# Kernel optimization log

Measured on AMD Instinct MI355X. Metric: run time of the kernel, lower is better.

Reference implementation:

```python
import jax, jax.numpy as jnp
import numpy as np

N_REP = 8      # N: repeated gelu(LN(linear)) blocks
M_LAYERS = 4   # M: transformer encoder layers
SEQ = 100
D = 4
FF = 2048      # PyTorch TransformerEncoderLayer default dim_feedforward
H = 4          # nhead; head_dim = 1


def _ln(x, g, b, axes):
    m = jnp.mean(x, axis=axes, keepdims=True)
    v = jnp.var(x, axis=axes, keepdims=True)
    return (x - m) / jnp.sqrt(v + 1e-5) * g + b


def _encoder_layer(x, Win, bi, Wout, bout, W1, b1, W2, b2, g1, be1, g2, be2):
    # x: [S, Nb, D] with S = batch_size (batch_first=False!), Nb = 100
    S, Nb, E = x.shape
    qkv = x @ Win.T + bi                      # [S, Nb, 3D]
    q, k, v = jnp.split(qkv, 3, axis=-1)
    qh = q.reshape(S, Nb, H, E // H)          # head_dim = 1, scale 1/sqrt(1)=1
    kh = k.reshape(S, Nb, H, E // H)
    vh = v.reshape(S, Nb, H, E // H)
    scores = jnp.einsum('snhd,tnhd->nhst', qh, kh)   # [Nb, H, S, S]
    attn = jax.nn.softmax(scores, axis=-1)
    o = jnp.einsum('nhst,tnhd->snhd', attn, vh).reshape(S, Nb, E)
    o = o @ Wout.T + bout
    x = _ln(x + o, g1, be1, (-1,))            # post-norm (norm_first=False)
    f = jax.nn.relu(x @ W1.T + b1) @ W2.T + b2
    return _ln(x + f, g2, be2, (-1,))


def setup_inputs() -> dict:
    key = jax.random.key(0)
    ks = jax.random.split(key, 24)
    B = 256
    d = {}
    d['x'] = jax.random.normal(ks[0], (B, SEQ, D), dtype=jnp.float32)
    # conv1: kernel_size=1, 1->1 channel -> scalar affine
    d['conv_w'] = jax.random.normal(ks[1], (), dtype=jnp.float32) * 0.5 + 1.0
    d['conv_b'] = jax.random.normal(ks[2], (), dtype=jnp.float32) * 0.1
    # shared 4x4 linear (self.liner) and LayerNorm([100,4])
    d['Wl'] = jax.random.normal(ks[3], (D, D), dtype=jnp.float32) * 0.5
    d['bl'] = jax.random.normal(ks[4], (D,), dtype=jnp.float32) * 0.1
    d['ln_g'] = jnp.ones((SEQ, D), dtype=jnp.float32)
    d['ln_b'] = jnp.zeros((SEQ, D), dtype=jnp.float32)
    # transformer encoder params, stacked over M layers
    s = 0.3
    d['Win'] = jax.random.normal(ks[5], (M_LAYERS, 3 * D, D), dtype=jnp.float32) * s
    d['bi'] = jax.random.normal(ks[6], (M_LAYERS, 3 * D), dtype=jnp.float32) * 0.05
    d['Wout'] = jax.random.normal(ks[7], (M_LAYERS, D, D), dtype=jnp.float32) * s
    d['bout'] = jax.random.normal(ks[8], (M_LAYERS, D), dtype=jnp.float32) * 0.05
    d['W1'] = jax.random.normal(ks[9], (M_LAYERS, FF, D), dtype=jnp.float32) * 0.05
    d['b1'] = jax.random.normal(ks[10], (M_LAYERS, FF), dtype=jnp.float32) * 0.05
    d['W2'] = jax.random.normal(ks[11], (M_LAYERS, D, FF), dtype=jnp.float32) * 0.02
    d['b2'] = jax.random.normal(ks[12], (M_LAYERS, D), dtype=jnp.float32) * 0.05
    d['g1'] = jnp.ones((M_LAYERS, D), dtype=jnp.float32)
    d['be1'] = jnp.zeros((M_LAYERS, D), dtype=jnp.float32)
    d['g2'] = jnp.ones((M_LAYERS, D), dtype=jnp.float32)
    d['be2'] = jnp.zeros((M_LAYERS, D), dtype=jnp.float32)
    return d


def reference(x, conv_w, conv_b, Wl, bl, ln_g, ln_b,
              Win, bi, Wout, bout, W1, b1, W2, b2, g1, be1, g2, be2):
    # per-channel kernel_size=1 conv == elementwise affine (same scalar for all 4 channels)
    h = x * conv_w + conv_b                   # [B, 100, 4]
    for _ in range(N_REP):
        h = jax.nn.gelu(_ln(h @ Wl.T + bl, ln_g, ln_b, (-2, -1)), approximate=False)
    h = h @ Wl.T + bl
    for i in range(M_LAYERS):
        h = _encoder_layer(h, Win[i], bi[i], Wout[i], bout[i], W1[i], b1[i],
                           W2[i], b2[i], g1[i], be1[i], g2[i], be2[i])
    h = h @ Wl.T + bl
    return jax.nn.softmax(h, axis=2)
```

## Files before the change

kernel.cpp:

```cpp
#include <hip/hip_runtime.h>
#include <math.h>

#define SEQ   100
#define BATCH 256
#define NREP  8
#define FFD   2048
#define RSQRT2 0.70710678118654752440f

__device__ __forceinline__ float wsum(float v) {
#pragma unroll
  for (int o = 32; o > 0; o >>= 1) v += __shfl_xor(v, o, 64);
  return v;
}

__global__ __launch_bounds__(256) void k_prep(
    const float* __restrict__ W2, float* __restrict__ W2T)
{
  const int id = blockIdx.x * 256 + threadIdx.x;
  const float* src = W2 + (id >> 11) * 4 * FFD + (id & 2047);
  *(float4*)(W2T + id * 4) =
      make_float4(src[0], src[FFD], src[2 * FFD], src[3 * FFD]);
}

__global__ __launch_bounds__(64) void k_stageA(
    const float* __restrict__ x, const float* __restrict__ convw,
    const float* __restrict__ convb, const float* __restrict__ Wl,
    const float* __restrict__ bl, const float* __restrict__ lng,
    const float* __restrict__ lnb, float* __restrict__ XT)
{
  const int b = blockIdx.x;
  const int lane = threadIdx.x;
  const bool act = lane < 50;

  const float cw = convw[0], cb = convb[0];
  float W[4][4], B[4];
#pragma unroll
  for (int j = 0; j < 4; ++j) {
    B[j] = bl[j];
#pragma unroll
    for (int d = 0; d < 4; ++d) W[j][d] = Wl[j * 4 + d];
  }
  float h[2][4] = {{0.f,0.f,0.f,0.f},{0.f,0.f,0.f,0.f}};
  float gg[2][4] = {{0.f}}, eb[2][4] = {{0.f}};
  if (act) {
#pragma unroll
    for (int p = 0; p < 2; ++p) {
      const int r = lane * 2 + p;
      float4 xr = *(const float4*)(x + (b * SEQ + r) * 4);
      h[p][0] = fmaf(xr.x, cw, cb); h[p][1] = fmaf(xr.y, cw, cb);
      h[p][2] = fmaf(xr.z, cw, cb); h[p][3] = fmaf(xr.w, cw, cb);
      float4 gv = *(const float4*)(lng + r * 4);
      float4 bv = *(const float4*)(lnb + r * 4);
      gg[p][0] = gv.x; gg[p][1] = gv.y; gg[p][2] = gv.z; gg[p][3] = gv.w;
      eb[p][0] = bv.x; eb[p][1] = bv.y; eb[p][2] = bv.z; eb[p][3] = bv.w;
    }
  }
  for (int it = 0; it < NREP; ++it) {
    float y[2][4] = {{0.f,0.f,0.f,0.f},{0.f,0.f,0.f,0.f}};
    float s1 = 0.f, s2 = 0.f;
    if (act) {
#pragma unroll
      for (int p = 0; p < 2; ++p)
#pragma unroll
        for (int j = 0; j < 4; ++j) {
          float yy = B[j];
#pragma unroll
          for (int d = 0; d < 4; ++d) yy = fmaf(h[p][d], W[j][d], yy);
          y[p][j] = yy; s1 += yy; s2 = fmaf(yy, yy, s2);
        }
    }
    s1 = wsum(s1); s2 = wsum(s2);
    const float mean = s1 * (1.0f / 400.0f);
    const float var  = s2 * (1.0f / 400.0f) - mean * mean;
    const float rstd = rsqrtf(var + 1e-5f);
    if (act) {
#pragma unroll
      for (int p = 0; p < 2; ++p)
#pragma unroll
        for (int j = 0; j < 4; ++j) {
          float vv = fmaf((y[p][j] - mean) * rstd, gg[p][j], eb[p][j]);
          h[p][j] = 0.5f * vv * (1.0f + erff(vv * RSQRT2));
        }
    }
  }
  if (act) {
#pragma unroll
    for (int p = 0; p < 2; ++p) {
      const int r = lane * 2 + p;
      float yy[4];
#pragma unroll
      for (int j = 0; j < 4; ++j) {
        float a = B[j];
#pragma unroll
        for (int d = 0; d < 4; ++d) a = fmaf(h[p][d], W[j][d], a);
        yy[j] = a;
      }
      *(float4*)(XT + (r * BATCH + b) * 4) =
          make_float4(yy[0], yy[1], yy[2], yy[3]);
    }
  }
}

__global__ __launch_bounds__(1024, 4) void k_layer(
    const float* __restrict__ XTin, float* __restrict__ XTout,
    const float* __restrict__ Wa,  const float* __restrict__ ba,
    const float* __restrict__ Wo,  const float* __restrict__ bo,
    const float* __restrict__ W1l, const float* __restrict__ b1l,
    const float* __restrict__ W2Tl,const float* __restrict__ b2l,
    const float* __restrict__ g1l, const float* __restrict__ e1l,
    const float* __restrict__ g2l, const float* __restrict__ e2l,
    const float* __restrict__ Wl,  const float* __restrict__ bl,
    float* __restrict__ out, const int last)
{
  const int n      = blockIdx.x;
  const int base_s = blockIdx.y * 128;
  const int t      = threadIdx.x;
  const int lane   = t & 63;
  const int wv     = t >> 6;
  const int ah     = wv & 3;
  const int kq     = wv >> 2;

  __shared__ __align__(16) float2 kv[4][256];
  __shared__ float2 part[4][128][5];
  __shared__ float  osm[4][128];
  __shared__ float  x1s[128][4];
  __shared__ float  fout[128][4];
  __shared__ float2 kred[4][4];

  {
    const int s = t & 255, hh = t >> 8;
    float4 xr = *(const float4*)(XTin + (n * BATCH + s) * 4);
    const float* wk = Wa + (4 + hh) * 4;
    const float* wp = Wa + (8 + hh) * 4;
    float k = ba[4+hh] + xr.x*wk[0] + xr.y*wk[1] + xr.z*wk[2] + xr.w*wk[3];
    float v = ba[8+hh] + xr.x*wp[0] + xr.y*wp[1] + xr.z*wp[2] + xr.w*wp[3];
    kv[hh][s] = make_float2(k, v);
  }
  float q0, q1;
  {
    const float* wq = Wa + ah * 4;
    float4 xa = *(const float4*)(XTin + (n * BATCH + base_s + 2 * lane) * 4);
    float4 xb = *(const float4*)(XTin + (n * BATCH + base_s + 2 * lane + 1) * 4);
    q0 = ba[ah] + xa.x*wq[0] + xa.y*wq[1] + xa.z*wq[2] + xa.w*wq[3];
    q1 = ba[ah] + xb.x*wq[0] + xb.y*wq[1] + xb.z*wq[2] + xb.w*wq[3];
  }
  __syncthreads();

  {
    float k = kv[ah][kq * 64 + lane].x;
    float mx = k, mn = k;
#pragma unroll
    for (int o = 32; o > 0; o >>= 1) {
      mx = fmaxf(mx, __shfl_xor(mx, o, 64));
      mn = fminf(mn, __shfl_xor(mn, o, 64));
    }
    if (lane == 0) kred[ah][kq] = make_float2(mx, mn);
  }
  __syncthreads();

  {
    const float kmx = fmaxf(fmaxf(kred[ah][0].x, kred[ah][1].x),
                            fmaxf(kred[ah][2].x, kred[ah][3].x));
    const float kmn = fminf(fminf(kred[ah][0].y, kred[ah][1].y),
                            fminf(kred[ah][2].y, kred[ah][3].y));
    const float m0 = (q0 >= 0.f) ? q0 * kmx : q0 * kmn;
    const float m1 = (q1 >= 0.f) ? q1 * kmx : q1 * kmn;
    const int kb = kq * 64;
    float dA = 0.f, nA = 0.f, dB = 0.f, nB = 0.f;
#pragma unroll 4
    for (int i = 0; i < 32; ++i) {
      const int p = ((lane + i) & 31) * 2;
      float4 kk = *(const float4*)&kv[ah][kb + p];
      float pA0 = __expf(fmaf(q0, kk.x, -m0));
      float pA1 = __expf(fmaf(q0, kk.z, -m0));
      float pB0 = __expf(fmaf(q1, kk.x, -m1));
      float pB1 = __expf(fmaf(q1, kk.z, -m1));
      dA += pA0 + pA1; nA = fmaf(pA1, kk.w, fmaf(pA0, kk.y, nA));
      dB += pB0 + pB1; nB = fmaf(pB1, kk.w, fmaf(pB0, kk.y, nB));
    }
    part[ah][2 * lane][kq]     = make_float2(dA, nA);
    part[ah][2 * lane + 1][kq] = make_float2(dB, nB);
  }
  __syncthreads();

  if (t < 512) {
    const int h = t >> 7, qr = t & 127;
    float2 a = part[h][qr][0], b = part[h][qr][1];
    float2 c = part[h][qr][2], d = part[h][qr][3];
    osm[h][qr] = (a.y + b.y + c.y + d.y) / (a.x + b.x + c.x + d.x);
  }
  __syncthreads();

  if (t < 512) {
    const int r = t >> 2, d = t & 3;
    const float o0 = osm[0][r], o1 = osm[1][r], o2 = osm[2][r], o3 = osm[3][r];
    float rr = XTin[(n * BATCH + base_s + r) * 4 + d] + bo[d]
             + o0*Wo[d*4+0] + o1*Wo[d*4+1] + o2*Wo[d*4+2] + o3*Wo[d*4+3];
    float sum = rr + __shfl_xor(rr, 1, 64); sum += __shfl_xor(sum, 2, 64);
    const float mean = 0.25f * sum;
    const float dv = rr - mean;
    float qq = dv * dv;
    float qs = qq + __shfl_xor(qq, 1, 64); qs += __shfl_xor(qs, 2, 64);
    const float rstd = rsqrtf(0.25f * qs + 1e-5f);
    x1s[r][d] = fmaf(dv * rstd, g1l[d], e1l[d]);
  }
  __syncthreads();

  {
    const int r0 = wv * 8;
    float xr[8][4];
#pragma unroll
    for (int rr = 0; rr < 8; ++rr) {
      float4 v = *(const float4*)&x1s[r0 + rr][0];
      xr[rr][0] = v.x; xr[rr][1] = v.y; xr[rr][2] = v.z; xr[rr][3] = v.w;
    }
    float acc[8][4] = {{0.f,0.f,0.f,0.f},{0.f,0.f,0.f,0.f},
                       {0.f,0.f,0.f,0.f},{0.f,0.f,0.f,0.f},
                       {0.f,0.f,0.f,0.f},{0.f,0.f,0.f,0.f},
                       {0.f,0.f,0.f,0.f},{0.f,0.f,0.f,0.f}};
    const float* w1p = W1l + lane * 4;
    const float* w2p = W2Tl + lane * 4;
    const float* b1p = b1l + lane;
#pragma unroll 4
    for (int j = 0; j < 32; ++j) {
      const float4 w1 = *(const float4*)(w1p + j * 256);
      const float4 w2 = *(const float4*)(w2p + j * 256);
      const float  bb = b1p[j * 64];
#pragma unroll
      for (int rr = 0; rr < 8; ++rr) {
        float hh = fmaf(xr[rr][3], w1.w, fmaf(xr[rr][2], w1.z,
                   fmaf(xr[rr][1], w1.y, fmaf(xr[rr][0], w1.x, bb))));
        hh = fmaxf(hh, 0.f);
        acc[rr][0] = fmaf(hh, w2.x, acc[rr][0]);
        acc[rr][1] = fmaf(hh, w2.y, acc[rr][1]);
        acc[rr][2] = fmaf(hh, w2.z, acc[rr][2]);
        acc[rr][3] = fmaf(hh, w2.w, acc[rr][3]);
      }
    }
#pragma unroll
    for (int rr = 0; rr < 8; ++rr)
#pragma unroll
      for (int d = 0; d < 4; ++d) {
        float v = acc[rr][d];
#pragma unroll
        for (int o = 32; o > 0; o >>= 1) v += __shfl_xor(v, o, 64);
        acc[rr][d] = v;
      }
    if (lane == 0) {
#pragma unroll
      for (int rr = 0; rr < 8; ++rr)
        *(float4*)&fout[r0 + rr][0] =
            make_float4(acc[rr][0], acc[rr][1], acc[rr][2], acc[rr][3]);
    }
  }
  __syncthreads();

  if (t < 512) {
    const int r = t >> 2, d = t & 3;
    float val = x1s[r][d] + fout[r][d] + b2l[d];
    float sum = val + __shfl_xor(val, 1, 64); sum += __shfl_xor(sum, 2, 64);
    const float mean = 0.25f * sum;
    const float dv = val - mean;
    float qq = dv * dv;
    float qs = qq + __shfl_xor(qq, 1, 64); qs += __shfl_xor(qs, 2, 64);
    const float rstd = rsqrtf(0.25f * qs + 1e-5f);
    const float res = fmaf(dv * rstd, g2l[d], e2l[d]);
    if (!last) XTout[(n * BATCH + base_s + r) * 4 + d] = res;
    else       x1s[r][d] = res;
  }

  if (last) {
    __syncthreads();
    if (t < 512) {
      const int r = t >> 2, j = t & 3;
      const float y = fmaf(x1s[r][3], Wl[j*4+3], fmaf(x1s[r][2], Wl[j*4+2],
                      fmaf(x1s[r][1], Wl[j*4+1], fmaf(x1s[r][0], Wl[j*4+0], bl[j]))));
      float mx = fmaxf(y, __shfl_xor(y, 1, 64)); mx = fmaxf(mx, __shfl_xor(mx, 2, 64));
      const float e = __expf(y - mx);
      float se = e + __shfl_xor(e, 1, 64); se += __shfl_xor(se, 2, 64);
      out[((base_s + r) * SEQ + n) * 4 + j] = e / se;
    }
  }
}

extern "C" void kernel_launch(void* const* d_in, const int* in_sizes, int n_in,
                              void* d_out, int out_size, void* d_ws, size_t ws_size,
                              hipStream_t stream)
{
  const float* x     = (const float*)d_in[0];
  const float* convw = (const float*)d_in[1];
  const float* convb = (const float*)d_in[2];
  const float* Wl    = (const float*)d_in[3];
  const float* bl    = (const float*)d_in[4];
  const float* lng   = (const float*)d_in[5];
  const float* lnb   = (const float*)d_in[6];
  const float* Win   = (const float*)d_in[7];
  const float* bi    = (const float*)d_in[8];
  const float* Wout  = (const float*)d_in[9];
  const float* bout  = (const float*)d_in[10];
  const float* W1    = (const float*)d_in[11];
  const float* b1    = (const float*)d_in[12];
  const float* W2    = (const float*)d_in[13];
  const float* b2    = (const float*)d_in[14];
  const float* g1    = (const float*)d_in[15];
  const float* be1   = (const float*)d_in[16];
  const float* g2    = (const float*)d_in[17];
  const float* be2   = (const float*)d_in[18];

  float* XT0 = (float*)d_ws;
  float* XT1 = XT0 + SEQ * BATCH * 4;
  float* W2T = XT1 + SEQ * BATCH * 4;

  k_prep<<<32, 256, 0, stream>>>(W2, W2T);
  k_stageA<<<BATCH, 64, 0, stream>>>(x, convw, convb, Wl, bl, lng, lnb, XT0);
  for (int l = 0; l < 4; ++l) {
    const float* in  = (l & 1) ? XT1 : XT0;
    float*       outb= (l & 1) ? XT0 : XT1;
    k_layer<<<dim3(SEQ, 2), 1024, 0, stream>>>(
        in, outb,
        Win + l * 48, bi + l * 12, Wout + l * 16, bout + l * 4,
        W1 + l * FFD * 4, b1 + l * FFD, W2T + l * FFD * 4, b2 + l * 4,
        g1 + l * 4, be1 + l * 4, g2 + l * 4, be2 + l * 4,
        Wl, bl, (float*)d_out, (l == 3) ? 1 : 0);
  }
}
```

Before: 134.1 us.

## Split FFN across waves by feature chunk with wave-uniform weights and LDS reduction

The FFN inner loop previously gave each wave 8 rows and had lanes stride over the hidden features, which ended in 32 cross-lane shuffle reductions per wave. Each wave now owns a 128-feature slice and each lane holds two rows. Weight addresses are wave-uniform (readfirstlane), so the compiler can issue scalar/broadcast loads. The 16 per-wave partial sums go to a larger shared buffer and are added in the LayerNorm step, which uses more LDS and may lower occupancy.

```diff
diff --git a/kernel.cpp b/kernel.cpp
--- a/kernel.cpp
+++ b/kernel.cpp
@@ -124,7 +124,7 @@
   __shared__ float2 part[4][128][5];
   __shared__ float  osm[4][128];
   __shared__ float  x1s[128][4];
-  __shared__ float  fout[128][4];
+  __shared__ float  pacc[16][128][4];
   __shared__ float2 kred[4][4];
 
   {
@@ -207,57 +207,52 @@
   __syncthreads();
 
   {
-    const int r0 = wv * 8;
-    float xr[8][4];
-#pragma unroll
-    for (int rr = 0; rr < 8; ++rr) {
-      float4 v = *(const float4*)&x1s[r0 + rr][0];
-      xr[rr][0] = v.x; xr[rr][1] = v.y; xr[rr][2] = v.z; xr[rr][3] = v.w;
-    }
-    float acc[8][4] = {{0.f,0.f,0.f,0.f},{0.f,0.f,0.f,0.f},
-                       {0.f,0.f,0.f,0.f},{0.f,0.f,0.f,0.f},
-                       {0.f,0.f,0.f,0.f},{0.f,0.f,0.f,0.f},
-                       {0.f,0.f,0.f,0.f},{0.f,0.f,0.f,0.f}};
-    const float* w1p = W1l + lane * 4;
-    const float* w2p = W2Tl + lane * 4;
-    const float* b1p = b1l + lane;
-#pragma unroll 4
-    for (int j = 0; j < 32; ++j) {
-      const float4 w1 = *(const float4*)(w1p + j * 256);
-      const float4 w2 = *(const float4*)(w2p + j * 256);
-      const float  bb = b1p[j * 64];
-#pragma unroll
-      for (int rr = 0; rr < 8; ++rr) {
-        float hh = fmaf(xr[rr][3], w1.w, fmaf(xr[rr][2], w1.z,
-                   fmaf(xr[rr][1], w1.y, fmaf(xr[rr][0], w1.x, bb))));
-        hh = fmaxf(hh, 0.f);
-        acc[rr][0] = fmaf(hh, w2.x, acc[rr][0]);
-        acc[rr][1] = fmaf(hh, w2.y, acc[rr][1]);
-        acc[rr][2] = fmaf(hh, w2.z, acc[rr][2]);
-        acc[rr][3] = fmaf(hh, w2.w, acc[rr][3]);
+    const int fb = __builtin_amdgcn_readfirstlane(wv) * 128;
+    const float* __restrict__ w1p = W1l  + fb * 4;
+    const float* __restrict__ w2p = W2Tl + fb * 4;
+    const float* __restrict__ b1p = b1l  + fb;
+    const float xA0 = x1s[lane][0],    xA1 = x1s[lane][1];
+    const float xA2 = x1s[lane][2],    xA3 = x1s[lane][3];
+    const float xB0 = x1s[64+lane][0], xB1 = x1s[64+lane][1];
+    const float xB2 = x1s[64+lane][2], xB3 = x1s[64+lane][3];
+    float aA0=0.f,aA1=0.f,aA2=0.f,aA3=0.f;
+    float aB0=0.f,aB1=0.f,aB2=0.f,aB3=0.f;
+#pragma unroll 2
+    for (int g = 0; g < 32; ++g) {
+      float w1v[16], w2v[16], bv[4];
+#pragma unroll
+      for (int i = 0; i < 16; ++i) w1v[i] = w1p[g * 16 + i];
+#pragma unroll
+      for (int i = 0; i < 16; ++i) w2v[i] = w2p[g * 16 + i];
+#pragma unroll
+      for (int i = 0; i < 4; ++i)  bv[i]  = b1p[g * 4 + i];
+#pragma unroll
+      for (int f = 0; f < 4; ++f) {
+        const float w10 = w1v[f*4+0], w11 = w1v[f*4+1];
+        const float w12 = w1v[f*4+2], w13 = w1v[f*4+3];
+        const float w20 = w2v[f*4+0], w21 = w2v[f*4+1];
+        const float w22 = w2v[f*4+2], w23 = w2v[f*4+3];
+        float hA = fmaf(xA3, w13, fmaf(xA2, w12, fmaf(xA1, w11, fmaf(xA0, w10, bv[f]))));
+        hA = fmaxf(hA, 0.f);
+        aA0 = fmaf(hA, w20, aA0); aA1 = fmaf(hA, w21, aA1);
+        aA2 = fmaf(hA, w22, aA2); aA3 = fmaf(hA, w23, aA3);
+        float hB = fmaf(xB3, w13, fmaf(xB2, w12, fmaf(xB1, w11, fmaf(xB0, w10, bv[f]))));
+        hB = fmaxf(hB, 0.f);
+        aB0 = fmaf(hB, w20, aB0); aB1 = fmaf(hB, w21, aB1);
+        aB2 = fmaf(hB, w22, aB2); aB3 = fmaf(hB, w23, aB3);
       }
     }
-#pragma unroll
-    for (int rr = 0; rr < 8; ++rr)
-#pragma unroll
-      for (int d = 0; d < 4; ++d) {
-        float v = acc[rr][d];
-#pragma unroll
-        for (int o = 32; o > 0; o >>= 1) v += __shfl_xor(v, o, 64);
-        acc[rr][d] = v;
-      }
-    if (lane == 0) {
-#pragma unroll
-      for (int rr = 0; rr < 8; ++rr)
-        *(float4*)&fout[r0 + rr][0] =
-            make_float4(acc[rr][0], acc[rr][1], acc[rr][2], acc[rr][3]);
-    }
+    *(float4*)&pacc[wv][lane][0]      = make_float4(aA0, aA1, aA2, aA3);
+    *(float4*)&pacc[wv][64 + lane][0] = make_float4(aB0, aB1, aB2, aB3);
   }
   __syncthreads();
 
   if (t < 512) {
     const int r = t >> 2, d = t & 3;
-    float val = x1s[r][d] + fout[r][d] + b2l[d];
+    float s16 = b2l[d];
+#pragma unroll
+    for (int w = 0; w < 16; ++w) s16 += pacc[w][r][d];
+    float val = x1s[r][d] + s16;
     float sum = val + __shfl_xor(val, 1, 64); sum += __shfl_xor(sum, 2, 64);
     const float mean = 0.25f * sum;
     const float dv = val - mean;
```

Measured after the change: 123.2 us. -8.1%, faster.
